# Optimization experiments

Measured on AMD Instinct MI355X. Metric: run time of the kernel, lower is better.

The kernel has to match this reference:

```python
import jax, jax.numpy as jnp
import numpy as np

B, T, A_DIM, Z_DIM, K = 128, 80, 32, 64, 16


def setup_inputs() -> dict:
    key = jax.random.key(0)
    k1, k2, k3, k4 = jax.random.split(key, 4)
    obs = jax.random.normal(k1, (B, T, A_DIM), jnp.float32)
    alpha_logits = jax.random.normal(k2, (B, T, K), jnp.float32)
    # torch init: A = eye(z) repeated K times; small noise keeps 80-step recursion stable
    A_K = jnp.eye(Z_DIM, dtype=jnp.float32)[None] + 0.005 * jax.random.normal(k3, (K, Z_DIM, Z_DIM), jnp.float32)
    # torch init: C = 0.05 * randn
    C_K = 0.05 * jax.random.normal(k4, (K, A_DIM, Z_DIM), jnp.float32)
    return {"obs": obs, "alpha_logits": alpha_logits, "A_K": A_K, "C_K": C_K}


def _kalman(obs, A, C):
    # obs [B,T,a], A [B,T,z,z], C [B,T,a,z]
    Bq, Tq, a_dim = obs.shape
    z_dim = A.shape[-1]
    dt = obs.dtype
    Q = 0.08 * jnp.eye(z_dim, dtype=dt)
    R = 0.03 * jnp.eye(a_dim, dtype=dt)
    I = jnp.eye(z_dim, dtype=dt)

    obs_t = jnp.swapaxes(obs, 0, 1)          # [T,B,a]
    A_t = jnp.swapaxes(A, 0, 1)              # [T,B,z,z]
    C_t = jnp.swapaxes(C, 0, 1)              # [T,B,a,z]
    A_next = jnp.concatenate([A_t[1:], A_t[-1:]], axis=0)  # A[t+1]; last unused

    mu0 = jnp.zeros((Bq, z_dim), dt)
    sig0 = jnp.broadcast_to(20.0 * I, (Bq, z_dim, z_dim))

    def filt_step(carry, inp):
        mu_p, sig_p, mu_prev = carry
        At, Anx, Ct, y = inp
        CtT = jnp.swapaxes(Ct, -1, -2)
        S = Ct @ sig_p @ CtT + R                       # [B,a,a]
        Kg = sig_p @ CtT @ jnp.linalg.inv(S)            # [B,z,a]
        Amu = jnp.einsum('bij,bj->bi', At, mu_prev)     # A_t mu_{t-1}
        err = y - jnp.einsum('bij,bj->bi', Ct, Amu)
        mu_f = Amu + jnp.einsum('bij,bj->bi', Kg, err)
        sig_f = (I - Kg @ Ct) @ sig_p
        mu_pn = jnp.einsum('bij,bj->bi', Anx, mu_f)     # prediction with A_{t+1}
        sig_pn = Anx @ sig_f @ jnp.swapaxes(Anx, -1, -2) + Q
        return (mu_pn, sig_pn, mu_f), (mu_f, sig_f, mu_p, sig_p)

    _, (mu_f, sig_f, mu_p, sig_p) = jax.lax.scan(
        filt_step, (mu0, sig0, mu0), (A_t, A_next, C_t, obs_t))

    def smooth_step(carry, inp):
        mu_s, sig_s = carry
        mf, sf, Anx, mpn, spn = inp
        J = sf @ jnp.swapaxes(Anx, -1, -2) @ jnp.linalg.inv(spn)
        mu = mf + jnp.einsum('bij,bj->bi', J, mu_s - mpn)
        sig = sf + J @ (sig_s - spn) @ jnp.swapaxes(J, -1, -2)
        return (mu, sig), (mu, sig)

    init = (mu_f[-1], sig_f[-1])
    _, (mu_sm, sig_sm) = jax.lax.scan(
        smooth_step, init,
        (mu_f[:-1], sig_f[:-1], A_t[1:], mu_p[1:], sig_p[1:]),
        reverse=True)
    mu_sm = jnp.concatenate([mu_sm, mu_f[-1:]], axis=0)
    sig_sm = jnp.concatenate([sig_sm, sig_f[-1:]], axis=0)
    return jnp.swapaxes(mu_sm, 0, 1), jnp.swapaxes(sig_sm, 0, 1)  # [B,T,z], [B,T,z,z]


def reference(obs, alpha_logits, A_K, C_K):
    w = jax.nn.softmax(alpha_logits, axis=-1)                # [B,T,K]
    A = jnp.einsum('btk,kij->btij', w, A_K)                  # [B,T,z,z]
    C = jnp.einsum('btk,kij->btij', w, C_K)                  # [B,T,a,z]
    return _kalman(obs, A, C)
```

## Files before the change

### kernel.cpp

```cpp
#include <hip/hip_runtime.h>

#define B_ 128
#define T_ 80
#define AD 32
#define ZD 64
#define KD 16
#define S8 68
#define SC 36

__device__ __forceinline__ float4 ld4(const float* p) { return *(const float4*)p; }
__device__ __forceinline__ void st4f(float* p, float4 v) { *(float4*)p = v; }
__device__ __forceinline__ float4 sub4(float4 a, float4 b) {
    return make_float4(a.x - b.x, a.y - b.y, a.z - b.z, a.w - b.w);
}
__device__ __forceinline__ float4 comb4(float4 c, float4 x0, float4 x1, float4 x2, float4 x3) {
    return make_float4(c.x*x0.x + c.y*x1.x + c.z*x2.x + c.w*x3.x,
                       c.x*x0.y + c.y*x1.y + c.z*x2.y + c.w*x3.y,
                       c.x*x0.z + c.y*x1.z + c.z*x2.z + c.w*x3.z,
                       c.x*x0.w + c.y*x1.w + c.z*x2.w + c.w*x3.w);
}

__device__ __forceinline__ float4 solve4(float4 q0, float4 q1, float4 q2, float4 q3, float4 f)
{
    float a01 = q1.x, a02 = q2.x, a03 = q3.x, b0 = f.x;
    float a11 = q1.y, a12 = q2.y, a13 = q3.y, b1 = f.y;
    float a21 = q1.z, a22 = q2.z, a23 = q3.z, b2 = f.z;
    float a31 = q1.w, a32 = q2.w, a33 = q3.w, b3 = f.w;
    const float r0 = 1.0f / q0.x;
    {
        const float m1 = q0.y * r0;
        a11 -= m1*a01; a12 -= m1*a02; a13 -= m1*a03; b1 -= m1*b0;
        const float m2 = q0.z * r0;
        a21 -= m2*a01; a22 -= m2*a02; a23 -= m2*a03; b2 -= m2*b0;
        const float m3 = q0.w * r0;
        a31 -= m3*a01; a32 -= m3*a02; a33 -= m3*a03; b3 -= m3*b0;
    }
    const float r1 = 1.0f / a11;
    {
        const float m2 = a21 * r1;
        a22 -= m2*a12; a23 -= m2*a13; b2 -= m2*b1;
        const float m3 = a31 * r1;
        a32 -= m3*a12; a33 -= m3*a13; b3 -= m3*b1;
    }
    const float r2 = 1.0f / a22;
    {
        const float m3 = a32 * r2;
        a33 -= m3*a23; b3 -= m3*b2;
    }
    const float x3 = b3 / a33;
    const float x2 = (b2 - a23*x3) * r2;
    const float x1 = (b1 - a13*x3 - a12*x2) * r1;
    const float x0 = (b0 - a03*x3 - a02*x2 - a01*x1) * r0;
    return make_float4(x0, x1, x2, x3);
}

template<int KL, int AS, int BS, bool ATRANS>
__device__ __forceinline__ void mm64(const float* __restrict__ Pa, const float* __restrict__ Qb,
                                     float acc[2][4], int r2, int c4)
{
#pragma unroll 8
    for (int k = 0; k < KL; k++) {
        float aA, aB;
        if (ATRANS) {
            const float2 av = *(const float2*)&Pa[k * AS + r2];
            aA = av.x; aB = av.y;
        } else {
            aA = Pa[r2 * AS + k]; aB = Pa[(r2 + 1) * AS + k];
        }
        const float4 bv = ld4(&Qb[k * BS + c4]);
        acc[0][0] += aA * bv.x; acc[0][1] += aA * bv.y; acc[0][2] += aA * bv.z; acc[0][3] += aA * bv.w;
        acc[1][0] += aB * bv.x; acc[1][1] += aB * bv.y; acc[1][2] += aB * bv.z; acc[1][3] += aB * bv.w;
    }
}

__global__ __launch_bounds__(512, 2)
void kvae_kernel(const float* __restrict__ obs, const float* __restrict__ logits,
                 const float* __restrict__ AK, const float* __restrict__ CK,
                 float* __restrict__ out)
{
    __shared__ __align__(16) float W[T_ * KD];
    __shared__ __align__(16) float Am[ZD * S8];
    __shared__ __align__(16) float At[ZD * S8];
    __shared__ __align__(16) float SP[ZD * S8];
    __shared__ __align__(16) float SF[ZD * S8];
    __shared__ __align__(16) float Mm[ZD * S8];
    __shared__ __align__(16) float Pool[9984];
    __shared__ __align__(16) float pvL[512];
    __shared__ __align__(16) float pvR[512];
    __shared__ __align__(16) float fbb[512];
    __shared__ __align__(16) float pvE[8];
    __shared__ __align__(16) float y_s[32];
    __shared__ __align__(16) float errv[32];
    __shared__ __align__(16) float uev[32];
    __shared__ __align__(16) float mup[64];
    __shared__ __align__(16) float muf[64];
    __shared__ __align__(16) float mus[64];
    __shared__ __align__(16) float mpn[64];
    __shared__ __align__(16) float dv[64];

    float* T1 = Pool;
    float* CM = Pool + 2176;
    float* CT = Pool + 4352;
    float* U_ = Pool + 6656;
    float* S_ = Pool + 8832;
    float* Xb = Pool;
    float* SG = Pool + 4352;

    const int tid = threadIdx.x;
    const int b   = blockIdx.x;

    const int r16 = tid >> 4;
    const int cg  = tid & 15;
    const int c4  = cg << 2;
    const int c2  = cg << 1;
    const int r2  = r16 << 1;
    const int gi  = tid >> 3;
    const int gs  = tid & 7;

    const float* obs_b = obs    + (size_t)b * T_ * AD;
    const float* lg_b  = logits + (size_t)b * T_ * KD;
    float* omu = out + (size_t)b * T_ * ZD;
    float* osg = out + (size_t)B_ * T_ * ZD + (size_t)b * T_ * ZD * ZD;
    const float4* AK4 = (const float4*)AK;
    const float4* CK4 = (const float4*)CK;

    auto mixA = [&](int tt) {
#pragma unroll
        for (int rr = 0; rr < 2; rr++) {
            const int r = r2 + rr;
            float4 a = make_float4(0.f, 0.f, 0.f, 0.f);
#pragma unroll
            for (int k = 0; k < KD; k++) {
                const float wk = W[tt * KD + k];
                const float4 v = AK4[k * 1024 + r * 16 + cg];
                a.x += wk * v.x; a.y += wk * v.y; a.z += wk * v.z; a.w += wk * v.w;
            }
            st4f(&Am[r * S8 + c4], a);
            At[(c4 + 0) * S8 + r] = a.x; At[(c4 + 1) * S8 + r] = a.y;
            At[(c4 + 2) * S8 + r] = a.z; At[(c4 + 3) * S8 + r] = a.w;
        }
    };
    auto mixC = [&](int tt) {
        float4 a = make_float4(0.f, 0.f, 0.f, 0.f);
#pragma unroll
        for (int k = 0; k < KD; k++) {
            const float wk = W[tt * KD + k];
            const float4 v = CK4[k * 512 + r16 * 16 + cg];
            a.x += wk * v.x; a.y += wk * v.y; a.z += wk * v.z; a.w += wk * v.w;
        }
        st4f(&CM[r16 * S8 + c4], a);
        CT[(c4 + 0) * SC + r16] = a.x; CT[(c4 + 1) * SC + r16] = a.y;
        CT[(c4 + 2) * SC + r16] = a.z; CT[(c4 + 3) * SC + r16] = a.w;
    };

    if (tid < T_) {
        float l[KD]; float mx = -1e30f;
#pragma unroll
        for (int k = 0; k < KD; k++) { l[k] = lg_b[tid * KD + k]; mx = fmaxf(mx, l[k]); }
        float s = 0.f;
#pragma unroll
        for (int k = 0; k < KD; k++) { l[k] = expf(l[k] - mx); s += l[k]; }
        const float inv = 1.0f / s;
#pragma unroll
        for (int k = 0; k < KD; k++) W[tid * KD + k] = l[k] * inv;
    }
#pragma unroll
    for (int rr = 0; rr < 2; rr++) {
        const int r = r2 + rr;
#pragma unroll
        for (int j = 0; j < 4; j++) SP[r * S8 + c4 + j] = (r == c4 + j) ? 20.0f : 0.0f;
    }
    if (tid < ZD) mup[tid] = 0.0f;
    __syncthreads();

    for (int t = 0; t < T_; t++) {
        if (t < T_ - 1) mixA(t + 1);
        mixC(t);
        if (tid < AD) y_s[tid] = obs_b[t * AD + tid];
        __syncthreads();

        {
            float a0 = 0, a1 = 0, a2 = 0, a3 = 0;
            const float* pa = CM + r16 * S8;
#pragma unroll 8
            for (int k = 0; k < ZD; k++) {
                const float a = pa[k];
                const float4 bv = ld4(&SP[k * S8 + c4]);
                a0 += a * bv.x; a1 += a * bv.y; a2 += a * bv.z; a3 += a * bv.w;
            }
            T1[r16 * S8 + c4 + 0] = a0; T1[r16 * S8 + c4 + 1] = a1;
            T1[r16 * S8 + c4 + 2] = a2; T1[r16 * S8 + c4 + 3] = a3;
        }
        __syncthreads();

        {
            float a0 = 0, a1 = 0;
            const float* pa = T1 + r16 * S8;
#pragma unroll 8
            for (int k = 0; k < ZD; k++) {
                const float a = pa[k];
                const float2 bv = *(const float2*)&CT[k * SC + c2];
                a0 += a * bv.x; a1 += a * bv.y;
            }
            if (r16 == c2)     a0 += 0.03f;
            if (r16 == c2 + 1) a1 += 0.03f;
            S_[r16 * SC + c2] = a0; S_[r16 * SC + c2 + 1] = a1;
            if (c2 < 4) { fbb[r16 * 4 + c2] = a0; fbb[r16 * 4 + c2 + 1] = a1; }
            if (r16 < 4) { pvL[r16 * 32 + c2] = a0; pvL[r16 * 32 + c2 + 1] = a1; }
        }
        if (tid < AD) {
            float s = 0.f;
#pragma unroll
            for (int k4 = 0; k4 < ZD; k4 += 4) {
                const float4 cm = ld4(&CM[tid * S8 + k4]);
                const float4 mu = ld4(&mup[k4]);
                s += cm.x*mu.x + cm.y*mu.y + cm.z*mu.z + cm.w*mu.w;
            }
            const float e_ = y_s[tid] - s;
            errv[tid] = e_;
            if (tid < 4) pvE[tid] = e_;
        }
        if (tid >= 448) {
            const int u = tid - 448; const int rr = u >> 4, cc = (u & 15) << 2;
            st4f(&pvR[rr * 64 + cc], ld4(&T1[rr * S8 + cc]));
        }
        __syncthreads();

        {
            const int hi = r16, hs = cg;
            float4 aL = make_float4(0, 0, 0, 0);
            float4 aR = ld4(&T1[hi * S8 + hs * 4]);
            float e = 0.f;
            if (hs < 8) aL = ld4(&S_[hi * SC + hs * 4]);
            if (hs == 15) e = errv[hi];

#pragma unroll 2
            for (int j = 0; j < 8; ++j) {
                const int par = j & 1, nb = par ^ 1;
                const bool isp = (hi >> 2) == j;
                const int i4 = hi & 3;
                const float4 q0 = ld4(&fbb[par * 128 + (4 * j + 0) * 4]);
                const float4 q1 = ld4(&fbb[par * 128 + (4 * j + 1) * 4]);
                const float4 q2 = ld4(&fbb[par * 128 + (4 * j + 2) * 4]);
                const float4 q3 = ld4(&fbb[par * 128 + (4 * j + 3) * 4]);
                float4 f;
                if (isp) f = make_float4(i4 == 0, i4 == 1, i4 == 2, i4 == 3);
                else     f = ld4(&fbb[par * 128 + hi * 4]);
                const float4 coef = solve4(q0, q1, q2, q3, f);
                {
                    const float4 c = comb4(coef,
                        ld4(&pvR[par * 256 + 0 * 64 + hs * 4]),
                        ld4(&pvR[par * 256 + 1 * 64 + hs * 4]),
                        ld4(&pvR[par * 256 + 2 * 64 + hs * 4]),
                        ld4(&pvR[par * 256 + 3 * 64 + hs * 4]));
                    if (isp) aR = c; else aR = sub4(aR, c);
                }
                if (hs < 8 && hs >= j) {
                    const float4 c = comb4(coef,
                        ld4(&pvL[par * 128 + 0 * 32 + hs * 4]),
                        ld4(&pvL[par * 128 + 1 * 32 + hs * 4]),
                        ld4(&pvL[par * 128 + 2 * 32 + hs * 4]),
                        ld4(&pvL[par * 128 + 3 * 32 + hs * 4]));
                    if (isp) aL = c; else aL = sub4(aL, c);
                }
                if (hs == 15) {
                    const float4 ev = ld4(&pvE[par * 4]);
                    const float ce = coef.x*ev.x + coef.y*ev.y + coef.z*ev.z + coef.w*ev.w;
                    if (isp) e = ce; else e -= ce;
                }
                if (j < 7) {
                    if ((hi >> 2) == j + 1) {
                        if (hs < 8 && hs >= j) st4f(&pvL[nb * 128 + i4 * 32 + hs * 4], aL);
                        st4f(&pvR[nb * 256 + i4 * 64 + hs * 4], aR);
                        if (hs == 15) pvE[nb * 4 + i4] = e;
                    }
                    if (hs == j + 1) st4f(&fbb[nb * 128 + hi * 4], aL);
                } else {
                    st4f(&U_[hi * S8 + hs * 4], aR);
                    if (hs == 15) uev[hi] = e;
                }
                __syncthreads();
            }
        }

        {
            float acc[2][4] = {};
            mm64<AD, S8, S8, true>(T1, U_, acc, r2, c4);
            float* og = osg + (size_t)t * ZD * ZD;
#pragma unroll
            for (int rr = 0; rr < 2; rr++) {
                const int r = r2 + rr;
                const float4 sp = ld4(&SP[r * S8 + c4]);
                const float4 v = make_float4(sp.x - acc[rr][0], sp.y - acc[rr][1],
                                             sp.z - acc[rr][2], sp.w - acc[rr][3]);
                st4f(&SF[r * S8 + c4], v);
                *(float4*)(og + r * ZD + c4) = v;
            }
        }
        if (tid < ZD) {
            float s = 0.f;
#pragma unroll
            for (int k = 0; k < AD; k++) s += T1[k * S8 + tid] * uev[k];
            const float v = mup[tid] + s;
            muf[tid] = v;
            omu[t * ZD + tid] = v;
        }
        __syncthreads();

        if (t < T_ - 1) {
            {
                float acc[2][4] = {};
                mm64<ZD, S8, S8, true>(At, SF, acc, r2, c4);
#pragma unroll
                for (int rr = 0; rr < 2; rr++)
                    st4f(&Mm[(r2 + rr) * S8 + c4],
                         make_float4(acc[rr][0], acc[rr][1], acc[rr][2], acc[rr][3]));
            }
            __syncthreads();
            {
                float acc[2][4] = {};
                mm64<ZD, S8, S8, false>(Mm, At, acc, r2, c4);
#pragma unroll
                for (int rr = 0; rr < 2; rr++) {
                    const int r = r2 + rr;
#pragma unroll
                    for (int j = 0; j < 4; j++)
                        SP[r * S8 + c4 + j] = acc[rr][j] + ((r == c4 + j) ? 0.08f : 0.0f);
                }
            }
            if (tid >= 448) {
                const int i = tid - 448;
                float s = 0.f;
                const float* pa = Am + i * S8;
#pragma unroll 8
                for (int k = 0; k < ZD; k++) s += pa[k] * muf[k];
                mup[i] = s;
            }
            __syncthreads();
        }
    }

#pragma unroll
    for (int rr = 0; rr < 2; rr++)
        st4f(&SG[(r2 + rr) * S8 + c4], ld4(&SF[(r2 + rr) * S8 + c4]));
    if (tid < ZD) mus[tid] = muf[tid];
    __syncthreads();

    for (int t = T_ - 2; t >= 0; t--) {
        mixA(t + 1);
        {
            const float4* og4 = (const float4*)(osg + (size_t)t * ZD * ZD);
#pragma unroll
            for (int rr = 0; rr < 2; rr++)
                st4f(&SF[(r2 + rr) * S8 + c4], og4[(r2 + rr) * 16 + cg]);
        }
        if (tid >= 448) muf[tid - 448] = omu[t * ZD + (tid - 448)];
        __syncthreads();

        {
            float acc[2][4] = {};
            mm64<ZD, S8, S8, true>(At, SF, acc, r2, c4);
#pragma unroll
            for (int rr = 0; rr < 2; rr++)
                st4f(&Mm[(r2 + rr) * S8 + c4],
                     make_float4(acc[rr][0], acc[rr][1], acc[rr][2], acc[rr][3]));
        }
        if (tid >= 448) {
            const int i = tid - 448;
            float s = 0.f;
            const float* pa = Am + i * S8;
#pragma unroll 8
            for (int k = 0; k < ZD; k++) s += pa[k] * muf[k];
            mpn[i] = s;
        }
        __syncthreads();

        {
            float acc[2][4] = {};
            mm64<ZD, S8, S8, false>(Mm, At, acc, r2, c4);
            float4 v0 = make_float4(acc[0][0] + ((r2 == c4 + 0) ? 0.08f : 0.0f),
                                    acc[0][1] + ((r2 == c4 + 1) ? 0.08f : 0.0f),
                                    acc[0][2] + ((r2 == c4 + 2) ? 0.08f : 0.0f),
                                    acc[0][3] + ((r2 == c4 + 3) ? 0.08f : 0.0f));
            float4 v1 = make_float4(acc[1][0] + ((r2 + 1 == c4 + 0) ? 0.08f : 0.0f),
                                    acc[1][1] + ((r2 + 1 == c4 + 1) ? 0.08f : 0.0f),
                                    acc[1][2] + ((r2 + 1 == c4 + 2) ? 0.08f : 0.0f),
                                    acc[1][3] + ((r2 + 1 == c4 + 3) ? 0.08f : 0.0f));
            st4f(&SP[r2 * S8 + c4], v0);
            st4f(&SP[(r2 + 1) * S8 + c4], v1);
            if (c4 == 0) { st4f(&fbb[r2 * 4], v0); st4f(&fbb[(r2 + 1) * 4], v1); }
            if (r2 < 4) {
                st4f(&pvL[r2 * 64 + c4], v0);
                st4f(&pvL[(r2 + 1) * 64 + c4], v1);
            }
        }
        if (tid >= 448) { const int i = tid - 448; dv[i] = mus[i] - mpn[i]; }
        if (tid < 64) {
            const int rr = tid >> 4, cc = (tid & 15) << 2;
            st4f(&pvR[rr * 64 + cc], ld4(&Mm[rr * S8 + cc]));
        }
        __syncthreads();

        {
            float4 aL0 = ld4(&SP[gi * S8 + gs * 8]);
            float4 aL1 = ld4(&SP[gi * S8 + gs * 8 + 4]);
            float4 aR0 = ld4(&Mm[gi * S8 + gs * 8]);
            float4 aR1 = ld4(&Mm[gi * S8 + gs * 8 + 4]);

#pragma unroll 2
            for (int j = 0; j < 16; ++j) {
                const int par = j & 1, nb = par ^ 1;
                const bool isp = (gi >> 2) == j;
                const int i4 = gi & 3;
                const float4 q0 = ld4(&fbb[par * 256 + (4 * j + 0) * 4]);
                const float4 q1 = ld4(&fbb[par * 256 + (4 * j + 1) * 4]);
                const float4 q2 = ld4(&fbb[par * 256 + (4 * j + 2) * 4]);
                const float4 q3 = ld4(&fbb[par * 256 + (4 * j + 3) * 4]);
                float4 f;
                if (isp) f = make_float4(i4 == 0, i4 == 1, i4 == 2, i4 == 3);
                else     f = ld4(&fbb[par * 256 + gi * 4]);
                const float4 coef = solve4(q0, q1, q2, q3, f);
                {
                    const float4 c0 = comb4(coef,
                        ld4(&pvR[par * 256 + 0 * 64 + gs * 8]),
                        ld4(&pvR[par * 256 + 1 * 64 + gs * 8]),
                        ld4(&pvR[par * 256 + 2 * 64 + gs * 8]),
                        ld4(&pvR[par * 256 + 3 * 64 + gs * 8]));
                    const float4 c1 = comb4(coef,
                        ld4(&pvR[par * 256 + 0 * 64 + gs * 8 + 4]),
                        ld4(&pvR[par * 256 + 1 * 64 + gs * 8 + 4]),
                        ld4(&pvR[par * 256 + 2 * 64 + gs * 8 + 4]),
                        ld4(&pvR[par * 256 + 3 * 64 + gs * 8 + 4]));
                    if (isp) { aR0 = c0; aR1 = c1; }
                    else     { aR0 = sub4(aR0, c0); aR1 = sub4(aR1, c1); }
                }
                if (2 * gs >= j) {
                    const float4 c0 = comb4(coef,
                        ld4(&pvL[par * 256 + 0 * 64 + gs * 8]),
                        ld4(&pvL[par * 256 + 1 * 64 + gs * 8]),
                        ld4(&pvL[par * 256 + 2 * 64 + gs * 8]),
                        ld4(&pvL[par * 256 + 3 * 64 + gs * 8]));
                    if (isp) aL0 = c0; else aL0 = sub4(aL0, c0);
                }
                if (2 * gs + 1 >= j) {
                    const float4 c1 = comb4(coef,
                        ld4(&pvL[par * 256 + 0 * 64 + gs * 8 + 4]),
                        ld4(&pvL[par * 256 + 1 * 64 + gs * 8 + 4]),
                        ld4(&pvL[par * 256 + 2 * 64 + gs * 8 + 4]),
                        ld4(&pvL[par * 256 + 3 * 64 + gs * 8 + 4]));
                    if (isp) aL1 = c1; else aL1 = sub4(aL1, c1);
                }
                if (j < 15) {
                    if ((gi >> 2) == j + 1) {
                        st4f(&pvR[nb * 256 + i4 * 64 + gs * 8], aR0);
                        st4f(&pvR[nb * 256 + i4 * 64 + gs * 8 + 4], aR1);
                        if (2 * gs >= j)     st4f(&pvL[nb * 256 + i4 * 64 + gs * 8], aL0);
                        if (2 * gs + 1 >= j) st4f(&pvL[nb * 256 + i4 * 64 + gs * 8 + 4], aL1);
                    }
                    if (gs == ((j + 1) >> 1))
                        st4f(&fbb[nb * 256 + gi * 4], ((j + 1) & 1) ? aL1 : aL0);
                } else {
                    st4f(&Xb[gi * S8 + gs * 8], aR0);
                    st4f(&Xb[gi * S8 + gs * 8 + 4], aR1);
                }
                __syncthreads();
            }
        }

        {
            float acc[2][4] = {};
            mm64<ZD, S8, S8, true>(SG, Xb, acc, r2, c4);
#pragma unroll
            for (int rr = 0; rr < 2; rr++) {
                const int r = r2 + rr;
                const float4 m = ld4(&Mm[r * S8 + c4]);
                SP[r * S8 + c4 + 0] = acc[rr][0] - m.x;
                SP[r * S8 + c4 + 1] = acc[rr][1] - m.y;
                SP[r * S8 + c4 + 2] = acc[rr][2] - m.z;
                SP[r * S8 + c4 + 3] = acc[rr][3] - m.w;
            }
        }
        __syncthreads();

        {
            float acc[2][4] = {};
            mm64<ZD, S8, S8, true>(Xb, SP, acc, r2, c4);
            float* og = osg + (size_t)t * ZD * ZD;
#pragma unroll
            for (int rr = 0; rr < 2; rr++) {
                const int r = r2 + rr;
                const float4 sf = ld4(&SF[r * S8 + c4]);
                const float4 v = make_float4(sf.x + acc[rr][0], sf.y + acc[rr][1],
                                             sf.z + acc[rr][2], sf.w + acc[rr][3]);
                st4f(&SG[r * S8 + c4], v);
                *(float4*)(og + r * ZD + c4) = v;
            }
        }
        if (tid < ZD) {
            float s = 0.f;
#pragma unroll 8
            for (int k = 0; k < ZD; k++) s += Xb[k * S8 + tid] * dv[k];
            const float v = muf[tid] + s;
            mus[tid] = v;
            omu[t * ZD + tid] = v;
        }
        __syncthreads();
    }
}

extern "C" void kernel_launch(void* const* d_in, const int* in_sizes, int n_in,
                              void* d_out, int out_size, void* d_ws, size_t ws_size,
                              hipStream_t stream) {
    const float* obs = (const float*)d_in[0];
    const float* lg  = (const float*)d_in[1];
    const float* AK  = (const float*)d_in[2];
    const float* CK  = (const float*)d_in[3];
    (void)d_ws; (void)ws_size; (void)in_sizes; (void)n_in; (void)out_size;
    kvae_kernel<<<dim3(B_), dim3(512), 0, stream>>>(obs, lg, AK, CK, (float*)d_out);
}
```

Before: 3.950 ms.

## Replace per-thread 4x4 Gaussian solve with block-inverse pivot and switch matmul operand forms

```diff
diff --git a/kernel.cpp b/kernel.cpp
--- a/kernel.cpp
+++ b/kernel.cpp
@@ -20,38 +20,29 @@
                        c.x*x0.w + c.y*x1.w + c.z*x2.w + c.w*x3.w);
 }
 
-__device__ __forceinline__ float4 solve4(float4 q0, float4 q1, float4 q2, float4 q3, float4 f)
+__device__ __forceinline__ void pinv4(float4 q0, float4 q1, float4 q2, float4 q3,
+                                      float4& pi0, float4& pi1, float4& pi2, float4& pi3)
 {
-    float a01 = q1.x, a02 = q2.x, a03 = q3.x, b0 = f.x;
-    float a11 = q1.y, a12 = q2.y, a13 = q3.y, b1 = f.y;
-    float a21 = q1.z, a22 = q2.z, a23 = q3.z, b2 = f.z;
-    float a31 = q1.w, a32 = q2.w, a33 = q3.w, b3 = f.w;
-    const float r0 = 1.0f / q0.x;
-    {
-        const float m1 = q0.y * r0;
-        a11 -= m1*a01; a12 -= m1*a02; a13 -= m1*a03; b1 -= m1*b0;
-        const float m2 = q0.z * r0;
-        a21 -= m2*a01; a22 -= m2*a02; a23 -= m2*a03; b2 -= m2*b0;
-        const float m3 = q0.w * r0;
-        a31 -= m3*a01; a32 -= m3*a02; a33 -= m3*a03; b3 -= m3*b0;
-    }
-    const float r1 = 1.0f / a11;
-    {
-        const float m2 = a21 * r1;
-        a22 -= m2*a12; a23 -= m2*a13; b2 -= m2*b1;
-        const float m3 = a31 * r1;
-        a32 -= m3*a12; a33 -= m3*a13; b3 -= m3*b1;
-    }
-    const float r2 = 1.0f / a22;
-    {
-        const float m3 = a32 * r2;
-        a33 -= m3*a23; b3 -= m3*b2;
-    }
-    const float x3 = b3 / a33;
-    const float x2 = (b2 - a23*x3) * r2;
-    const float x1 = (b1 - a13*x3 - a12*x2) * r1;
-    const float x0 = (b0 - a03*x3 - a02*x2 - a01*x1) * r0;
-    return make_float4(x0, x1, x2, x3);
+    const float ra = 1.0f / (q0.x*q1.y - q0.y*q1.x);
+    const float ai00 =  q1.y*ra, ai01 = -q0.y*ra, ai10 = -q1.x*ra, ai11 = q0.x*ra;
+    const float ca00 = q2.x*ai00 + q2.y*ai10, ca01 = q2.x*ai01 + q2.y*ai11;
+    const float ca10 = q3.x*ai00 + q3.y*ai10, ca11 = q3.x*ai01 + q3.y*ai11;
+    const float s00 = q2.z - (ca00*q0.z + ca01*q1.z), s01 = q2.w - (ca00*q0.w + ca01*q1.w);
+    const float s10 = q3.z - (ca10*q0.z + ca11*q1.z), s11 = q3.w - (ca10*q0.w + ca11*q1.w);
+    const float rs = 1.0f / (s00*s11 - s01*s10);
+    const float si00 = s11*rs, si01 = -s01*rs, si10 = -s10*rs, si11 = s00*rs;
+    const float ab00 = ai00*q0.z + ai01*q1.z, ab01 = ai00*q0.w + ai01*q1.w;
+    const float ab10 = ai10*q0.z + ai11*q1.z, ab11 = ai10*q0.w + ai11*q1.w;
+    const float t00 = ab00*si00 + ab01*si10, t01 = ab00*si01 + ab01*si11;
+    const float t10 = ab10*si00 + ab11*si10, t11 = ab10*si01 + ab11*si11;
+    const float tl00 = ai00 + (t00*ca00 + t01*ca10), tl01 = ai01 + (t00*ca01 + t01*ca11);
+    const float tl10 = ai10 + (t10*ca00 + t11*ca10), tl11 = ai11 + (t10*ca01 + t11*ca11);
+    const float bl00 = -(si00*ca00 + si01*ca10), bl01 = -(si00*ca01 + si01*ca11);
+    const float bl10 = -(si10*ca00 + si11*ca10), bl11 = -(si10*ca01 + si11*ca11);
+    pi0 = make_float4(tl00, tl01, -t00, -t01);
+    pi1 = make_float4(tl10, tl11, -t10, -t11);
+    pi2 = make_float4(bl00, bl01, si00, si01);
+    pi3 = make_float4(bl10, bl11, si10, si11);
 }
 
 template<int KL, int AS, int BS, bool ATRANS>
@@ -61,12 +52,8 @@
 #pragma unroll 8
     for (int k = 0; k < KL; k++) {
         float aA, aB;
-        if (ATRANS) {
-            const float2 av = *(const float2*)&Pa[k * AS + r2];
-            aA = av.x; aB = av.y;
-        } else {
-            aA = Pa[r2 * AS + k]; aB = Pa[(r2 + 1) * AS + k];
-        }
+        if (ATRANS) { aA = Pa[k * AS + r2];   aB = Pa[k * AS + r2 + 1]; }
+        else        { aA = Pa[r2 * AS + k];   aB = Pa[(r2 + 1) * AS + k]; }
         const float4 bv = ld4(&Qb[k * BS + c4]);
         acc[0][0] += aA * bv.x; acc[0][1] += aA * bv.y; acc[0][2] += aA * bv.z; acc[0][3] += aA * bv.w;
         acc[1][0] += aB * bv.x; acc[1][1] += aB * bv.y; acc[1][2] += aB * bv.z; acc[1][3] += aB * bv.w;
@@ -243,10 +230,14 @@
                 const float4 q1 = ld4(&fbb[par * 128 + (4 * j + 1) * 4]);
                 const float4 q2 = ld4(&fbb[par * 128 + (4 * j + 2) * 4]);
                 const float4 q3 = ld4(&fbb[par * 128 + (4 * j + 3) * 4]);
-                float4 f;
-                if (isp) f = make_float4(i4 == 0, i4 == 1, i4 == 2, i4 == 3);
-                else     f = ld4(&fbb[par * 128 + hi * 4]);
-                const float4 coef = solve4(q0, q1, q2, q3, f);
+                float4 pi0, pi1, pi2, pi3;
+                pinv4(q0, q1, q2, q3, pi0, pi1, pi2, pi3);
+                float4 coef;
+                if (isp) coef = (i4 == 0 ? pi0 : i4 == 1 ? pi1 : i4 == 2 ? pi2 : pi3);
+                else {
+                    const float4 f = ld4(&fbb[par * 128 + hi * 4]);
+                    coef = comb4(f, pi0, pi1, pi2, pi3);
+                }
                 {
                     const float4 c = comb4(coef,
                         ld4(&pvR[par * 256 + 0 * 64 + hs * 4]),
@@ -310,7 +301,7 @@
         if (t < T_ - 1) {
             {
                 float acc[2][4] = {};
-                mm64<ZD, S8, S8, true>(At, SF, acc, r2, c4);
+                mm64<ZD, S8, S8, false>(Am, SF, acc, r2, c4);
 #pragma unroll
                 for (int rr = 0; rr < 2; rr++)
                     st4f(&Mm[(r2 + rr) * S8 + c4],
@@ -359,7 +350,7 @@
 
         {
             float acc[2][4] = {};
-            mm64<ZD, S8, S8, true>(At, SF, acc, r2, c4);
+            mm64<ZD, S8, S8, false>(Am, SF, acc, r2, c4);
 #pragma unroll
             for (int rr = 0; rr < 2; rr++)
                 st4f(&Mm[(r2 + rr) * S8 + c4],
@@ -416,10 +407,14 @@
                 const float4 q1 = ld4(&fbb[par * 256 + (4 * j + 1) * 4]);
                 const float4 q2 = ld4(&fbb[par * 256 + (4 * j + 2) * 4]);
                 const float4 q3 = ld4(&fbb[par * 256 + (4 * j + 3) * 4]);
-                float4 f;
-                if (isp) f = make_float4(i4 == 0, i4 == 1, i4 == 2, i4 == 3);
-                else     f = ld4(&fbb[par * 256 + gi * 4]);
-                const float4 coef = solve4(q0, q1, q2, q3, f);
+                float4 pi0, pi1, pi2, pi3;
+                pinv4(q0, q1, q2, q3, pi0, pi1, pi2, pi3);
+                float4 coef;
+                if (isp) coef = (i4 == 0 ? pi0 : i4 == 1 ? pi1 : i4 == 2 ? pi2 : pi3);
+                else {
+                    const float4 f = ld4(&fbb[par * 256 + gi * 4]);
+                    coef = comb4(f, pi0, pi1, pi2, pi3);
+                }
                 {
                     const float4 c0 = comb4(coef,
                         ld4(&pvR[par * 256 + 0 * 64 + gs * 8]),
@@ -469,7 +464,7 @@
 
         {
             float acc[2][4] = {};
-            mm64<ZD, S8, S8, true>(SG, Xb, acc, r2, c4);
+            mm64<ZD, S8, S8, false>(SG, Xb, acc, r2, c4);
 #pragma unroll
             for (int rr = 0; rr < 2; rr++) {
                 const int r = r2 + rr;
```

After: 3.722 ms. 5.8% less time.
